# Kernel optimization log

Hardware: AMD Instinct MI355X
Metric: run time of the kernel (lower is better)

The kernel has to match this reference:

```python
import jax, jax.numpy as jnp
import numpy as np

L1, L2, N, C = 4096, 4096, 8, 3


def setup_inputs() -> dict:
    key = jax.random.key(0)
    k1, k2 = jax.random.split(key)
    coords1 = jax.random.uniform(k1, (L1, N, C), dtype=jnp.float32)
    coords2 = jax.random.uniform(k2, (L2, N, C), dtype=jnp.float32)
    return {"coords1": coords1, "coords2": coords2}


def reference(coords1, coords2):
    # coords1: [L1, N, C], coords2: [L2, N, C]
    l1, n, c = coords1.shape
    l2 = coords2.shape[0]
    # Batch-first layout, matching flatten_batch semantics (per-batch NN only)
    q = jnp.swapaxes(coords2, 0, 1)  # [N, L2, C] query points
    r = jnp.swapaxes(coords1, 0, 1)  # [N, L1, C] reference points
    # Squared euclidean distances per batch: [N, L2, L1]
    d2 = (
        jnp.sum(q * q, axis=-1)[:, :, None]
        + jnp.sum(r * r, axis=-1)[:, None, :]
        - 2.0 * jnp.einsum("nlc,nmc->nlm", q, r)
    )
    # tc.nearest returns global flat index; original does fmod(L1) to get the
    # per-batch index — argmin within each batch gives that directly.
    nearest = jnp.argmin(d2, axis=-1)  # [N, L2]
    clusters = nearest.T  # [L2, N]
    # torch.meshgrid(arange(L2), arange(N)) with 'ij' indexing; indices[-1] is
    # the batch index broadcast to [L2, N].
    batch_idx = jnp.broadcast_to(jnp.arange(n, dtype=jnp.int64 if False else jnp.int32), (l2, n))
    return (clusters.reshape(-1), batch_idx.reshape(-1))
```

## Files before the change

kernel.cpp:

```cpp
#include <hip/hip_runtime.h>
#include <float.h>
#include <limits.h>


constexpr int kL1 = 4096, kL2 = 4096, kN = 8;
constexpr int kCS = 520;
constexpr size_t kOffCurR = 8ull * kCS * 4;
constexpr size_t kOffCsQ  = kOffCurR + 8ull * 512 * 4;
constexpr size_t kOffCurQ = kOffCsQ + 8ull * kCS * 4;
constexpr size_t kOffCellR = kOffCurQ + 8ull * 512 * 4;
constexpr size_t kOffCellQ = kOffCellR + 32768ull * 2;
constexpr size_t kOffPtsR = kOffCellQ + 32768ull * 2;
constexpr size_t kOffPtsQ = kOffPtsR + 8ull * 4096 * 16;
constexpr size_t kWsBytes = kOffPtsQ + 8ull * 4096 * 16;

__device__ __forceinline__ float rr_exact(float x, float y, float z) {
  return __fadd_rn(__fadd_rn(__fmul_rn(x, x), __fmul_rn(y, y)), __fmul_rn(z, z));
}

__device__ __forceinline__ int cell_of(float x, float y, float z) {
  const int cx = min(7, max(0, (int)(x * 8.0f)));
  const int cy = min(7, max(0, (int)(y * 8.0f)));
  const int cz = min(7, max(0, (int)(z * 8.0f)));
  return (cz * 8 + cy) * 8 + cx;
}

__global__ __launch_bounds__(256)
void cellof_kernel(const float* __restrict__ c1, const float* __restrict__ c2,
                   unsigned short* __restrict__ cellR,
                   unsigned short* __restrict__ cellQ) {
  const int t = blockIdx.x * 256 + threadIdx.x;
  const int u = t & 32767;
  const float* p = (t < 32768 ? c1 : c2) + 3 * u;
  const int c = cell_of(p[0], p[1], p[2]);
  if (t < 32768) cellR[u] = (unsigned short)c;
  else cellQ[u] = (unsigned short)c;
}

__global__ __launch_bounds__(1024)
void histscan_kernel(const unsigned short* __restrict__ cellR,
                     const unsigned short* __restrict__ cellQ,
                     int* __restrict__ csR, int* __restrict__ curR,
                     int* __restrict__ csQ, int* __restrict__ curQ) {
  __shared__ int hist[512];
  const int tid = threadIdx.x;
  const int n = blockIdx.x & 7;
  const bool isQ = blockIdx.x >= 8;
  const unsigned short* cof = isQ ? cellQ : cellR;
  int* cs = isQ ? csQ : csR;
  int* cur = isQ ? curQ : curR;
  if (tid < 512) hist[tid] = 0;
  __syncthreads();

#pragma unroll
  for (int k = 0; k < 4; ++k) {
    const int j = k * 1024 + tid;
    atomicAdd(&hist[cof[j * kN + n]], 1);
  }
  __syncthreads();

  if (tid < 64) {
    int loc[8], part = 0;
#pragma unroll
    for (int i = 0; i < 8; ++i) { loc[i] = hist[tid * 8 + i]; part += loc[i]; }
    int inc = part;
#pragma unroll
    for (int off = 1; off < 64; off <<= 1) {
      const int v = __shfl_up(inc, off);
      if (tid >= off) inc += v;
    }
    int base = inc - part;
#pragma unroll
    for (int i = 0; i < 8; ++i) {
      const int c = tid * 8 + i;
      cs[n * kCS + c] = base;
      cur[n * 512 + c] = base;
      base += loc[i];
    }
    if (tid == 0) cs[n * kCS + 512] = 4096;
  }
}

__global__ __launch_bounds__(256)
void scatter_kernel(const float* __restrict__ c1, const float* __restrict__ c2,
                    const unsigned short* __restrict__ cellR,
                    const unsigned short* __restrict__ cellQ,
                    int* __restrict__ curR, int* __restrict__ curQ,
                    float4* __restrict__ ptsR, float4* __restrict__ ptsQ) {
  const int t = blockIdx.x * 256 + threadIdx.x;
  const int u = t & 32767;
  const bool isQ = t >= 32768;
  const float* p = (isQ ? c2 : c1) + 3 * u;
  const float x = p[0], y = p[1], z = p[2];
  const int n = u & 7, j = u >> 3;
  const int cell = (isQ ? cellQ : cellR)[u];
  int* cur = isQ ? curQ : curR;
  float4* pts = isQ ? ptsQ : ptsR;
  const int pos = atomicAdd(&cur[n * 512 + cell], 1);
  pts[n * 4096 + pos] = make_float4(x, y, z, __int_as_float(j));
}

__global__ __launch_bounds__(128)
void cell_nn_kernel(const int* __restrict__ csR, const float4* __restrict__ ptsR,
                    const float4* __restrict__ ptsQ, int* __restrict__ out) {
#pragma clang fp contract(off)
  const int n = blockIdx.y;
  const int qslot = blockIdx.x * 32 + (threadIdx.x >> 2);
  const int sub = threadIdx.x & 3;

  const float4 qp = ptsQ[n * 4096 + qslot];
  const float qx = qp.x, qy = qp.y, qz = qp.z;
  const float qq = rr_exact(qx, qy, qz);
  const int cx = min(7, max(0, (int)(qx * 8.0f)));
  const int cy = min(7, max(0, (int)(qy * 8.0f)));
  const int cz = min(7, max(0, (int)(qz * 8.0f)));
  const int xlo = max(0, cx - 1), xhi = min(7, cx + 1);

  const int* __restrict__ cs = csR + n * kCS;
  const float4* __restrict__ P = ptsR + n * 4096;

  float bd = FLT_MAX;
  int bi = INT_MAX;

#pragma unroll
  for (int k = 0; k < 9; ++k) {
    const int dz = k / 3 - 1, dy = k % 3 - 1;
    const int z = cz + dz, y = cy + dy;
    const bool valid = ((unsigned)z <= 7u) && ((unsigned)y <= 7u);
    const int zc = min(7, max(0, z)), yc = min(7, max(0, y));
    const int row = (zc * 8 + yc) * 8;
    const int s = cs[row + xlo];
    const int e = valid ? cs[row + xhi + 1] : s;
    for (int p = s + sub; p < e; p += 4) {
      const float4 rp = P[p];
      const int id = __float_as_int(rp.w);
      const float rr = rr_exact(rp.x, rp.y, rp.z);
      const float dot = __fadd_rn(
          __fadd_rn(__fmul_rn(qx, rp.x), __fmul_rn(qy, rp.y)),
          __fmul_rn(qz, rp.z));
      const float d2 = __fmaf_rn(-2.0f, dot, __fadd_rn(qq, rr));
      if (d2 < bd || (d2 == bd && id < bi)) { bd = d2; bi = id; }
    }
  }

#pragma unroll
  for (int m = 1; m <= 2; m <<= 1) {
    const float od = __shfl_xor(bd, m);
    const int oi = __shfl_xor(bi, m);
    if (od < bd || (od == bd && oi < bi)) { bd = od; bi = oi; }
  }

  if (!(0.015625f > __fadd_rn(bd, 4e-6f))) {
    for (int p = sub; p < kL1; p += 4) {
      const float4 rp = P[p];
      const int id = __float_as_int(rp.w);
      const float rr = rr_exact(rp.x, rp.y, rp.z);
      const float dot = __fadd_rn(
          __fadd_rn(__fmul_rn(qx, rp.x), __fmul_rn(qy, rp.y)),
          __fmul_rn(qz, rp.z));
      const float d2 = __fmaf_rn(-2.0f, dot, __fadd_rn(qq, rr));
      if (d2 < bd || (d2 == bd && id < bi)) { bd = d2; bi = id; }
    }
#pragma unroll
    for (int m = 1; m <= 2; m <<= 1) {
      const float od = __shfl_xor(bd, m);
      const int oi = __shfl_xor(bi, m);
      if (od < bd || (od == bd && oi < bi)) { bd = od; bi = oi; }
    }
  }

  if (sub == 0) {
    const int qj = __float_as_int(qp.w);
    out[qj * kN + n] = bi;
    out[kL2 * kN + qj * kN + n] = n;
  }
}

constexpr int kQPerBlock = 16;
constexpr int kQ = 4;
constexpr int kChunk = 1024;

__global__ __launch_bounds__(256, 4)
void nearest_kernel_lds(const float* __restrict__ c1, const float* __restrict__ c2,
                        int* __restrict__ out) {
#pragma clang fp contract(off)
  __shared__ float sRx[kChunk], sRy[kChunk], sRz[kChunk], sRr[kChunk];
  const int tid = threadIdx.x;
  const int n = blockIdx.y;
  const int wave = tid >> 6;
  const int lane = tid & 63;
  const int q0 = blockIdx.x * kQPerBlock + wave * kQ;

  float qxs[kQ], qys[kQ], qzs[kQ], qqs[kQ];
#pragma unroll
  for (int i = 0; i < kQ; ++i) {
    const float* p = c2 + ((q0 + i) * kN + n) * 3;
    qxs[i] = p[0]; qys[i] = p[1]; qzs[i] = p[2];
    qqs[i] = rr_exact(qxs[i], qys[i], qzs[i]);
  }
  float bd[kQ]; int bt[kQ];
#pragma unroll
  for (int i = 0; i < kQ; ++i) { bd[i] = FLT_MAX; bt[i] = 0; }

  for (int chunk = 0; chunk < kL1 / kChunk; ++chunk) {
    __syncthreads();
    {
      const int jb = chunk * kChunk + tid * 4;
      float x[4], y[4], z[4], w4[4];
#pragma unroll
      for (int k = 0; k < 4; ++k) {
        const float* p = c1 + ((jb + k) * kN + n) * 3;
        x[k] = p[0]; y[k] = p[1]; z[k] = p[2];
        w4[k] = rr_exact(x[k], y[k], z[k]);
      }
      *reinterpret_cast<float4*>(&sRx[tid * 4]) = make_float4(x[0], x[1], x[2], x[3]);
      *reinterpret_cast<float4*>(&sRy[tid * 4]) = make_float4(y[0], y[1], y[2], y[3]);
      *reinterpret_cast<float4*>(&sRz[tid * 4]) = make_float4(z[0], z[1], z[2], z[3]);
      *reinterpret_cast<float4*>(&sRr[tid * 4]) = make_float4(w4[0], w4[1], w4[2], w4[3]);
    }
    __syncthreads();
#pragma unroll
    for (int t = 0; t < kChunk / 256; ++t) {
      const int tg = chunk * (kChunk / 256) + t;
      const int base = t * 256 + lane * 4;
      const float4 x4 = *reinterpret_cast<const float4*>(&sRx[base]);
      const float4 y4 = *reinterpret_cast<const float4*>(&sRy[base]);
      const float4 z4 = *reinterpret_cast<const float4*>(&sRz[base]);
      const float4 r4 = *reinterpret_cast<const float4*>(&sRr[base]);
      const float xs[4] = {x4.x, x4.y, x4.z, x4.w};
      const float ys[4] = {y4.x, y4.y, y4.z, y4.w};
      const float zs[4] = {z4.x, z4.y, z4.z, z4.w};
      const float rs[4] = {r4.x, r4.y, r4.z, r4.w};
#pragma unroll
      for (int i = 0; i < kQ; ++i) {
        float d[4];
#pragma unroll
        for (int k = 0; k < 4; ++k) {
          const float dot = __fadd_rn(
              __fadd_rn(__fmul_rn(qxs[i], xs[k]), __fmul_rn(qys[i], ys[k])),
              __fmul_rn(qzs[i], zs[k]));
          d[k] = __fmaf_rn(-2.0f, dot, __fadd_rn(qqs[i], rs[k]));
        }
        const float old = bd[i];
        float m = fminf(fminf(d[0], d[1]), old);
        m = fminf(fminf(d[2], d[3]), m);
        bd[i] = m;
        if (m < old) bt[i] = tg;
      }
    }
  }
  int sel[kQ];
#pragma unroll
  for (int i = 0; i < kQ; ++i) sel[i] = bt[i] * 64 + lane;
#pragma unroll
  for (int m = 1; m <= 32; m <<= 1) {
#pragma unroll
    for (int i = 0; i < kQ; ++i) {
      const float od = __shfl_xor(bd[i], m);
      const int os = __shfl_xor(sel[i], m);
      if (od < bd[i] || (od == bd[i] && os < sel[i])) { bd[i] = od; sel[i] = os; }
    }
  }
#pragma unroll
  for (int i = 0; i < kQ; ++i) {
    if (lane == i) {
      const int j0 = sel[i] * 4;
      float best = FLT_MAX; int kk = 0;
#pragma unroll
      for (int k = 0; k < 4; ++k) {
        const float* p = c1 + ((j0 + k) * kN + n) * 3;
        const float r0 = p[0], r1 = p[1], r2 = p[2];
        const float rr = rr_exact(r0, r1, r2);
        const float dot = __fadd_rn(
            __fadd_rn(__fmul_rn(qxs[i], r0), __fmul_rn(qys[i], r1)),
            __fmul_rn(qzs[i], r2));
        const float dc = __fmaf_rn(-2.0f, dot, __fadd_rn(qqs[i], rr));
        if (dc < best) { best = dc; kk = k; }
      }
      out[(q0 + i) * kN + n] = j0 + kk;
      out[kL2 * kN + (q0 + i) * kN + n] = n;
    }
  }
}

extern "C" void kernel_launch(void* const* d_in, const int* in_sizes, int n_in,
                              void* d_out, int out_size, void* d_ws, size_t ws_size,
                              hipStream_t stream) {
  const float* c1 = (const float*)d_in[0];
  const float* c2 = (const float*)d_in[1];
  int* out = (int*)d_out;
  if (d_ws != nullptr && ws_size >= kWsBytes) {
    int* csR = (int*)d_ws;
    int* curR = (int*)((char*)d_ws + kOffCurR);
    int* csQ = (int*)((char*)d_ws + kOffCsQ);
    int* curQ = (int*)((char*)d_ws + kOffCurQ);
    unsigned short* cellR = (unsigned short*)((char*)d_ws + kOffCellR);
    unsigned short* cellQ = (unsigned short*)((char*)d_ws + kOffCellQ);
    float4* ptsR = (float4*)((char*)d_ws + kOffPtsR);
    float4* ptsQ = (float4*)((char*)d_ws + kOffPtsQ);
    cellof_kernel<<<dim3(256), dim3(256), 0, stream>>>(c1, c2, cellR, cellQ);
    histscan_kernel<<<dim3(16), dim3(1024), 0, stream>>>(cellR, cellQ, csR, curR,
                                                         csQ, curQ);
    scatter_kernel<<<dim3(256), dim3(256), 0, stream>>>(c1, c2, cellR, cellQ,
                                                        curR, curQ, ptsR, ptsQ);
    cell_nn_kernel<<<dim3(128, 8), dim3(128), 0, stream>>>(csR, ptsR, ptsQ, out);
  } else {
    dim3 grid(kL2 / kQPerBlock, kN);
    nearest_kernel_lds<<<grid, dim3(256), 0, stream>>>(c1, c2, out);
  }
}
```

Measured before the change: 88.07 us.

## Process queries per grid cell with shared LDS-staged neighbor candidates

Replaces the per-query cell search kernel with one block per (batch, query cell). Each block gathers the reference points of the 3x3x3 neighborhood into LDS once, and every wave then scans them for up to eight queries at a time, so candidate loads are reused across all queries in the cell instead of refetched per query. The cost is more block-level synchronisation and many mostly-empty or tiny blocks (4096 blocks, about 8 queries per cell on average). Lanes are also underused when a cell has few queries, and the brute-force fallback now runs per wave with 64 lanes.

```diff
diff --git a/kernel.cpp b/kernel.cpp
--- a/kernel.cpp
+++ b/kernel.cpp
@@ -100,28 +100,28 @@
   pts[n * 4096 + pos] = make_float4(x, y, z, __int_as_float(j));
 }
 
-__global__ __launch_bounds__(128)
-void cell_nn_kernel(const int* __restrict__ csR, const float4* __restrict__ ptsR,
-                    const float4* __restrict__ ptsQ, int* __restrict__ out) {
+constexpr int kMaxR = 8;
+constexpr int kCand = 1024;
+
+__global__ __launch_bounds__(256)
+void cellblock_nn_kernel(const int* __restrict__ csRall, const int* __restrict__ csQall,
+                         const float4* __restrict__ ptsR,
+                         const float4* __restrict__ ptsQ, int* __restrict__ out) {
 #pragma clang fp contract(off)
-  const int n = blockIdx.y;
-  const int qslot = blockIdx.x * 32 + (threadIdx.x >> 2);
-  const int sub = threadIdx.x & 3;
-
-  const float4 qp = ptsQ[n * 4096 + qslot];
-  const float qx = qp.x, qy = qp.y, qz = qp.z;
-  const float qq = rr_exact(qx, qy, qz);
-  const int cx = min(7, max(0, (int)(qx * 8.0f)));
-  const int cy = min(7, max(0, (int)(qy * 8.0f)));
-  const int cz = min(7, max(0, (int)(qz * 8.0f)));
+  __shared__ float4 cand[kCand];
+  const int bx = blockIdx.x;
+  const int n = bx & 7, cell = bx >> 3;
+  const int tid = threadIdx.x, wave = tid >> 6, lane = tid & 63;
+  const int qs = csQall[n * kCS + cell], qe = csQall[n * kCS + cell + 1];
+  if (qs >= qe) return;
+
+  const int cx = cell & 7, cy = (cell >> 3) & 7, cz = cell >> 6;
   const int xlo = max(0, cx - 1), xhi = min(7, cx + 1);
-
-  const int* __restrict__ cs = csR + n * kCS;
-  const float4* __restrict__ P = ptsR + n * 4096;
-
-  float bd = FLT_MAX;
-  int bi = INT_MAX;
-
+  const int* __restrict__ cs = csRall + n * kCS;
+  const float4* __restrict__ PR = ptsR + n * 4096;
+  const float4* __restrict__ PQ = ptsQ + n * 4096;
+
+  int S[9], Lk[9], pre[10];
 #pragma unroll
   for (int k = 0; k < 9; ++k) {
     const int dz = k / 3 - 1, dy = k % 3 - 1;
@@ -130,49 +130,102 @@
     const int zc = min(7, max(0, z)), yc = min(7, max(0, y));
     const int row = (zc * 8 + yc) * 8;
     const int s = cs[row + xlo];
-    const int e = valid ? cs[row + xhi + 1] : s;
-    for (int p = s + sub; p < e; p += 4) {
-      const float4 rp = P[p];
-      const int id = __float_as_int(rp.w);
-      const float rr = rr_exact(rp.x, rp.y, rp.z);
-      const float dot = __fadd_rn(
-          __fadd_rn(__fmul_rn(qx, rp.x), __fmul_rn(qy, rp.y)),
-          __fmul_rn(qz, rp.z));
-      const float d2 = __fmaf_rn(-2.0f, dot, __fadd_rn(qq, rr));
-      if (d2 < bd || (d2 == bd && id < bi)) { bd = d2; bi = id; }
-    }
-  }
-
-#pragma unroll
-  for (int m = 1; m <= 2; m <<= 1) {
-    const float od = __shfl_xor(bd, m);
-    const int oi = __shfl_xor(bi, m);
-    if (od < bd || (od == bd && oi < bi)) { bd = od; bi = oi; }
-  }
-
-  if (!(0.015625f > __fadd_rn(bd, 4e-6f))) {
-    for (int p = sub; p < kL1; p += 4) {
-      const float4 rp = P[p];
-      const int id = __float_as_int(rp.w);
-      const float rr = rr_exact(rp.x, rp.y, rp.z);
-      const float dot = __fadd_rn(
-          __fadd_rn(__fmul_rn(qx, rp.x), __fmul_rn(qy, rp.y)),
-          __fmul_rn(qz, rp.z));
-      const float d2 = __fmaf_rn(-2.0f, dot, __fadd_rn(qq, rr));
-      if (d2 < bd || (d2 == bd && id < bi)) { bd = d2; bi = id; }
-    }
-#pragma unroll
-    for (int m = 1; m <= 2; m <<= 1) {
-      const float od = __shfl_xor(bd, m);
-      const int oi = __shfl_xor(bi, m);
-      if (od < bd || (od == bd && oi < bi)) { bd = od; bi = oi; }
-    }
-  }
-
-  if (sub == 0) {
-    const int qj = __float_as_int(qp.w);
-    out[qj * kN + n] = bi;
-    out[kL2 * kN + qj * kN + n] = n;
+    const int e = cs[row + xhi + 1];
+    S[k] = s;
+    Lk[k] = valid ? (e - s) : 0;
+  }
+  pre[0] = 0;
+#pragma unroll
+  for (int k = 0; k < 9; ++k) pre[k + 1] = pre[k] + Lk[k];
+  const int T = pre[9];
+
+  for (int qg = qs; qg < qe; qg += 4 * kMaxR) {
+    float qx[kMaxR], qy[kMaxR], qz[kMaxR], qq[kMaxR], bd[kMaxR];
+    int bi[kMaxR];
+#pragma unroll
+    for (int r = 0; r < kMaxR; ++r) {
+      bd[r] = FLT_MAX; bi[r] = INT_MAX;
+      const int q = qg + wave + 4 * r;
+      if (q < qe) {
+        const float4 qp = PQ[q];
+        qx[r] = qp.x; qy[r] = qp.y; qz[r] = qp.z;
+        qq[r] = rr_exact(qp.x, qp.y, qp.z);
+      }
+    }
+
+    for (int cb = 0; cb < T; cb += kCand) {
+      const int tc = min(kCand, T - cb);
+      __syncthreads();
+#pragma unroll
+      for (int u = 0; u < 4; ++u) {
+        const int sl = tid + 256 * u;
+        if (sl < tc) {
+          const int g = cb + sl;
+          int ad = 0;
+#pragma unroll
+          for (int k = 0; k < 9; ++k) {
+            const bool in = (g >= pre[k]) && (g < pre[k + 1]);
+            ad = in ? (S[k] + (g - pre[k])) : ad;
+          }
+          cand[sl] = PR[ad];
+        }
+      }
+      __syncthreads();
+
+#pragma unroll
+      for (int r = 0; r < kMaxR; ++r) {
+        const int q = qg + wave + 4 * r;
+        if (q < qe) {
+          for (int i = lane; i < tc; i += 64) {
+            const float4 rp = cand[i];
+            const int id = __float_as_int(rp.w);
+            const float rr = rr_exact(rp.x, rp.y, rp.z);
+            const float dot = __fadd_rn(
+                __fadd_rn(__fmul_rn(qx[r], rp.x), __fmul_rn(qy[r], rp.y)),
+                __fmul_rn(qz[r], rp.z));
+            const float d2 = __fmaf_rn(-2.0f, dot, __fadd_rn(qq[r], rr));
+            if (d2 < bd[r] || (d2 == bd[r] && id < bi[r])) { bd[r] = d2; bi[r] = id; }
+          }
+        }
+      }
+    }
+
+#pragma unroll
+    for (int r = 0; r < kMaxR; ++r) {
+      const int q = qg + wave + 4 * r;
+      if (q < qe) {
+        float bdr = bd[r]; int bir = bi[r];
+#pragma unroll
+        for (int m = 1; m <= 32; m <<= 1) {
+          const float od = __shfl_xor(bdr, m);
+          const int oi = __shfl_xor(bir, m);
+          if (od < bdr || (od == bdr && oi < bir)) { bdr = od; bir = oi; }
+        }
+        if (!(0.015625f > __fadd_rn(bdr, 4e-6f))) {
+          for (int pp = lane; pp < kL1; pp += 64) {
+            const float4 rp = PR[pp];
+            const int id = __float_as_int(rp.w);
+            const float rr = rr_exact(rp.x, rp.y, rp.z);
+            const float dot = __fadd_rn(
+                __fadd_rn(__fmul_rn(qx[r], rp.x), __fmul_rn(qy[r], rp.y)),
+                __fmul_rn(qz[r], rp.z));
+            const float d2 = __fmaf_rn(-2.0f, dot, __fadd_rn(qq[r], rr));
+            if (d2 < bdr || (d2 == bdr && id < bir)) { bdr = d2; bir = id; }
+          }
+#pragma unroll
+          for (int m = 1; m <= 32; m <<= 1) {
+            const float od = __shfl_xor(bdr, m);
+            const int oi = __shfl_xor(bir, m);
+            if (od < bdr || (od == bdr && oi < bir)) { bdr = od; bir = oi; }
+          }
+        }
+        if (lane == 0) {
+          const int qj = __float_as_int(PQ[q].w);
+          out[qj * kN + n] = bir;
+          out[kL2 * kN + qj * kN + n] = n;
+        }
+      }
+    }
   }
 }
 
@@ -303,7 +356,8 @@
                                                          csQ, curQ);
     scatter_kernel<<<dim3(256), dim3(256), 0, stream>>>(c1, c2, cellR, cellQ,
                                                         curR, curQ, ptsR, ptsQ);
-    cell_nn_kernel<<<dim3(128, 8), dim3(128), 0, stream>>>(csR, ptsR, ptsQ, out);
+    cellblock_nn_kernel<<<dim3(4096), dim3(256), 0, stream>>>(csR, csQ, ptsR,
+                                                              ptsQ, out);
   } else {
     dim3 grid(kL2 / kQPerBlock, kN);
     nearest_kernel_lds<<<grid, dim3(256), 0, stream>>>(c1, c2, out);
```

After: 98.61 us. 1.12x slower.
